# Kernel optimization log

Hardware: AMD Instinct MI355X
Metric: run time of the kernel (lower is better)

## Reference

```python
import jax, jax.numpy as jnp
import numpy as np

DIM = 1536
NH = 24
HD = DIM // NH
EPS = 1e-5


def _ln(x, gamma):
    # LayerNorm over last dim (head_dim), affine weight only, no bias
    mu = jnp.mean(x, axis=-1, keepdims=True)
    var = jnp.var(x, axis=-1, keepdims=True)
    return (x - mu) * jax.lax.rsqrt(var + EPS) * gamma


def setup_inputs() -> dict:
    key = jax.random.key(0)
    ks = jax.random.split(key, 24)
    B, S, T = 1, 2048, 512
    std = 0.02
    d = {
        "hidden_states": jax.random.normal(ks[0], (B, S, DIM), jnp.float32),
        "encoder_hidden_states": jax.random.normal(ks[1], (B, T, DIM), jnp.float32),
        "Wq": jax.random.normal(ks[2], (DIM, DIM), jnp.float32) * std,
        "bq": jnp.zeros((DIM,), jnp.float32),
        "Wk": jax.random.normal(ks[3], (DIM, DIM), jnp.float32) * std,
        "bk": jnp.zeros((DIM,), jnp.float32),
        "Wv": jax.random.normal(ks[4], (DIM, DIM), jnp.float32) * std,
        "bv": jnp.zeros((DIM,), jnp.float32),
        "Waq": jax.random.normal(ks[5], (DIM, DIM), jnp.float32) * std,
        "baq": jnp.zeros((DIM,), jnp.float32),
        "Wak": jax.random.normal(ks[6], (DIM, DIM), jnp.float32) * std,
        "bak": jnp.zeros((DIM,), jnp.float32),
        "Wav": jax.random.normal(ks[7], (DIM, DIM), jnp.float32) * std,
        "bav": jnp.zeros((DIM,), jnp.float32),
        "Wo": jax.random.normal(ks[8], (DIM, DIM), jnp.float32) * std,
        "bo": jnp.zeros((DIM,), jnp.float32),
        "Wao": jax.random.normal(ks[9], (DIM, DIM), jnp.float32) * std,
        "bao": jnp.zeros((DIM,), jnp.float32),
        "gq": jnp.ones((HD,), jnp.float32),
        "gk": jnp.ones((HD,), jnp.float32),
        "gaq": jnp.ones((HD,), jnp.float32),
        "gak": jnp.ones((HD,), jnp.float32),
    }
    return d


def reference(hidden_states, encoder_hidden_states, Wq, bq, Wk, bk, Wv, bv,
              Waq, baq, Wak, bak, Wav, bav, Wo, bo, Wao, bao, gq, gk, gaq, gak):
    B, S, _ = hidden_states.shape
    T = encoder_hidden_states.shape[1]

    def proj(x, W, b):
        # nn.Linear: x @ W.T + b ; reshape to (B, L, NH, HD)
        y = jnp.einsum('bld,ed->ble', x, W) + b
        return y.reshape(B, -1, NH, HD)

    q = _ln(proj(hidden_states, Wq, bq), gq)
    k = _ln(proj(hidden_states, Wk, bk), gk)
    v = proj(hidden_states, Wv, bv)
    eq = _ln(proj(encoder_hidden_states, Waq, baq), gaq)
    ek = _ln(proj(encoder_hidden_states, Wak, bak), gak)
    ev = proj(encoder_hidden_states, Wav, bav)

    q_cat = jnp.concatenate([q, eq], axis=1)  # (B, S+T, H, D)
    k_cat = jnp.concatenate([k, ek], axis=1)
    v_cat = jnp.concatenate([v, ev], axis=1)

    scale = 1.0 / np.sqrt(HD).astype(np.float32)
    scores = jnp.einsum('bqhd,bkhd->bhqk', q_cat, k_cat) * scale
    attn = jax.nn.softmax(scores, axis=-1)
    out = jnp.einsum('bhqk,bkhd->bqhd', attn, v_cat).reshape(B, S + T, DIM)

    img_out = jnp.einsum('bld,ed->ble', out[:, :S], Wo) + bo
    txt_out = jnp.einsum('bld,ed->ble', out[:, S:], Wao) + bao
    return (img_out, txt_out)
```

## Files before the change

kernel.cpp:

```cpp
#include <hip/hip_runtime.h>

#define DIMD 1536
#define LTOT 2560
#define NS 2048
#define NT 512

typedef __bf16 bf16x8 __attribute__((ext_vector_type(8)));
typedef float f32x4 __attribute__((ext_vector_type(4)));
typedef int i32x2 __attribute__((ext_vector_type(2)));
typedef unsigned short u16;
typedef unsigned int u32;

__device__ __forceinline__ u16 f2bf(float f) {
  union { float f; unsigned u; } v; v.f = f;
  return (u16)((v.u + 0x7fffu + ((v.u >> 16) & 1u)) >> 16);
}

__device__ __forceinline__ u32 cvt_pk_bf16(float a, float b) {
  u32 r;
  asm("v_cvt_pk_bf16_f32 %0, %1, %2" : "=v"(r) : "v"(a), "v"(b));
  return r;
}

__device__ __forceinline__ void gload_lds16(const void* g, void* l) {
  __builtin_amdgcn_global_load_lds(
      (__attribute__((address_space(1))) void*)(g),
      (__attribute__((address_space(3))) void*)(l), 16, 0, 0);
}

struct CvtArgs {
  const float* src[10];
  u16* dst[10];
  int n[10];
};

__global__ __launch_bounds__(256) void cvt_all(CvtArgs a) {
  const int seg = blockIdx.y;
  const int n = a.n[seg];
  const float* s = a.src[seg];
  u16* d = a.dst[seg];
  const int i = (blockIdx.x * 256 + threadIdx.x) * 4;
  if (i < n) {
    float4 v = *reinterpret_cast<const float4*>(s + i);
    ushort4 o;
    o.x = f2bf(v.x); o.y = f2bf(v.y); o.z = f2bf(v.z); o.w = f2bf(v.w);
    *reinterpret_cast<ushort4*>(d + i) = o;
  }
}


__device__ __forceinline__ void gemm_stage(const u16* pA, const u16* pW,
                                           u16* As, u16* Bs, int wo) {
#pragma unroll
  for (int p = 0; p < 2; ++p) {
    gload_lds16(pA + (long)p * 64 * DIMD, As + p * 2048 + wo);
    gload_lds16(pW + (long)p * 64 * DIMD, Bs + p * 2048 + wo);
  }
}

__device__ __forceinline__ void gemm_compute(
    const u16* As, const u16* Bs, f32x4 (&acc)[4][4],
    int wr, int wc, int l15, int lh) {
  bf16x8 af[4], bfr[4];
#pragma unroll
  for (int m = 0; m < 4; ++m)
    af[m] = *reinterpret_cast<const bf16x8*>(As + (wr + m * 16 + l15) * 32 + lh * 8);
#pragma unroll
  for (int n = 0; n < 4; ++n)
    bfr[n] = *reinterpret_cast<const bf16x8*>(Bs + (wc + n * 16 + l15) * 32 + lh * 8);
#pragma unroll
  for (int m = 0; m < 4; ++m)
#pragma unroll
    for (int n = 0; n < 4; ++n)
      acc[m][n] = __builtin_amdgcn_mfma_f32_16x16x32_bf16(af[m], bfr[n], acc[m][n], 0, 0, 0);
}

__device__ __forceinline__ void gemm_mainloop(
    const u16* __restrict__ A, const u16* __restrict__ W,
    u16* As0, u16* Bs0, u16* As1, u16* Bs1, f32x4 (&acc)[4][4],
    int w, int lane, int wr, int wc, int l15, int lh) {
  const int base = w * 64 + lane;
  const u16* pA = A + (long)(base >> 2) * DIMD + (base & 3) * 8;
  const u16* pW = W + (long)(base >> 2) * DIMD + (base & 3) * 8;
  const int wo = w * 512;

  gemm_stage(pA, pW, As0, Bs0, wo); pA += 32; pW += 32;
  for (int k0 = 0; k0 < DIMD; k0 += 64) {
    gemm_stage(pA, pW, As1, Bs1, wo); pA += 32; pW += 32;
    asm volatile("s_waitcnt vmcnt(4)" ::: "memory");
    __builtin_amdgcn_s_barrier();
    gemm_compute(As0, Bs0, acc, wr, wc, l15, lh);
    __builtin_amdgcn_s_barrier();
    if (k0 + 64 < DIMD) {
      gemm_stage(pA, pW, As0, Bs0, wo); pA += 32; pW += 32;
      asm volatile("s_waitcnt vmcnt(4)" ::: "memory");
    } else {
      asm volatile("s_waitcnt vmcnt(0)" ::: "memory");
    }
    __builtin_amdgcn_s_barrier();
    gemm_compute(As1, Bs1, acc, wr, wc, l15, lh);
    __builtin_amdgcn_s_barrier();
  }
}

struct QkvArgs {
  const u16* xb; const u16* exb;
  const u16* w[6];
  const float* b[6];
  const float* g[4];
  u16* qcat; u16* kcat; u16* vcat;
};

__global__ __launch_bounds__(256) void qkv_gemm(QkvArgs a) {
  __shared__ u16 As0[128 * 32];
  __shared__ u16 Bs0[128 * 32];
  __shared__ u16 As1[128 * 32];
  __shared__ u16 Bs1[128 * 32];
  const int tid = threadIdx.x, lane = tid & 63, w = tid >> 6;
  const int l15 = lane & 15, lh = lane >> 4;
  const int side = (blockIdx.x >= 16);
  const int mb = side ? (blockIdx.x - 16) : blockIdx.x;
  const int sel = blockIdx.y / 12;
  const int n0 = (blockIdx.y % 12) * 128;
  const long m0 = (long)mb * 128;
  const long Lbase = side ? NS : 0;
  const int wr = (w >> 1) * 64, wc = (w & 1) * 64;
  const u16* A = (side ? a.exb : a.xb) + m0 * DIMD;
  const u16* W = a.w[side * 3 + sel] + (long)n0 * DIMD;
  const float* bias = a.b[side * 3 + sel];

  f32x4 acc[4][4] = {};
  gemm_mainloop(A, W, As0, Bs0, As1, Bs1, acc, w, lane, wr, wc, l15, lh);

  if (sel == 2) {
    u16* out = a.vcat;
#pragma unroll
    for (int m = 0; m < 4; ++m)
#pragma unroll
      for (int r = 0; r < 4; ++r) {
        const long row = Lbase + m0 + wr + m * 16 + lh * 4 + r;
#pragma unroll
        for (int n = 0; n < 4; ++n)
          out[row * DIMD + n0 + wc + n * 16 + l15] =
              f2bf(acc[m][n][r] + bias[n0 + wc + n * 16 + l15]);
      }
  } else {
    const float* gamma = a.g[side * 2 + sel];
    const float gscale = (sel == 0) ? 0.125f * 1.4426950408889634f : 1.0f;
    u16* out = (sel == 0) ? a.qcat : a.kcat;
    const int swz = (sel == 1);
#pragma unroll
    for (int m = 0; m < 4; ++m) {
      float val[4][4];
#pragma unroll
      for (int n = 0; n < 4; ++n) {
        const float b = bias[n0 + wc + n * 16 + l15];
#pragma unroll
        for (int r = 0; r < 4; ++r) val[n][r] = acc[m][n][r] + b;
      }
      float s1[4], s2[4];
#pragma unroll
      for (int r = 0; r < 4; ++r) {
        s1[r] = 0.f; s2[r] = 0.f;
#pragma unroll
        for (int n = 0; n < 4; ++n) { s1[r] += val[n][r]; s2[r] += val[n][r] * val[n][r]; }
      }
#pragma unroll
      for (int off = 1; off < 16; off <<= 1) {
#pragma unroll
        for (int r = 0; r < 4; ++r) {
          s1[r] += __shfl_xor(s1[r], off, 16);
          s2[r] += __shfl_xor(s2[r], off, 16);
        }
      }
#pragma unroll
      for (int r = 0; r < 4; ++r) {
        const float mu = s1[r] * (1.0f / 64.0f);
        const float var = s2[r] * (1.0f / 64.0f) - mu * mu;
        const float rstd = rsqrtf(var + 1e-5f);
        const long row = Lbase + m0 + wr + m * 16 + lh * 4 + r;
        const int r7s = ((lh * 4 + r) & 7) << 3;
#pragma unroll
        for (int n = 0; n < 4; ++n) {
          const float g = gamma[n * 16 + l15] * gscale;
          const int colg = n0 + wc + n * 16 + l15;
          const int colstore = swz ? ((colg & ~63) | ((colg & 63) ^ r7s)) : colg;
          out[row * DIMD + colstore] = f2bf((val[n][r] - mu) * rstd * g);
        }
      }
    }
  }
}

struct OutArgs {
  const u16* aout;
  const u16* w[2];
  const float* b[2];
  float* out;
};

__global__ __launch_bounds__(256) void out_gemm(OutArgs a) {
  __shared__ u16 As0[128 * 32];
  __shared__ u16 Bs0[128 * 32];
  __shared__ u16 As1[128 * 32];
  __shared__ u16 Bs1[128 * 32];
  const int tid = threadIdx.x, lane = tid & 63, w = tid >> 6;
  const int l15 = lane & 15, lh = lane >> 4;
  const int side = (blockIdx.x >= 16);
  const int mb = side ? (blockIdx.x - 16) : blockIdx.x;
  const int n0 = blockIdx.y * 128;
  const long m0 = (long)mb * 128;
  const long Lbase = side ? NS : 0;
  const int wr = (w >> 1) * 64, wc = (w & 1) * 64;
  const u16* A = a.aout + (Lbase + m0) * DIMD;
  const u16* W = a.w[side] + (long)n0 * DIMD;
  const float* bias = a.b[side];

  f32x4 acc[4][4] = {};
  gemm_mainloop(A, W, As0, Bs0, As1, Bs1, acc, w, lane, wr, wc, l15, lh);

#pragma unroll
  for (int m = 0; m < 4; ++m)
#pragma unroll
    for (int r = 0; r < 4; ++r) {
      const long row = Lbase + m0 + wr + m * 16 + lh * 4 + r;
#pragma unroll
      for (int n = 0; n < 4; ++n)
        a.out[row * DIMD + n0 + wc + n * 16 + l15] =
            acc[m][n][r] + bias[n0 + wc + n * 16 + l15];
    }
}

__global__ __launch_bounds__(256) void vtrans(const u16* __restrict__ vcat,
                                              u16* __restrict__ VT) {
  const int tid = threadIdx.x;
  const int kv0 = blockIdx.x * 64;
  const int head = blockIdx.y;
  const long hb = (long)head * 64;
#pragma unroll
  for (int p = 0; p < 2; ++p) {
    const int idx = p * 256 + tid;
    const int kl = idx >> 3, db = (idx & 7) * 8;
    uint4 vv = *reinterpret_cast<const uint4*>(vcat + (long)(kv0 + kl) * DIMD + hb + db);
    const u16* vs = reinterpret_cast<const u16*>(&vv);
#pragma unroll
    for (int i = 0; i < 8; ++i) {
      const int d = db + i;
      VT[(hb + d) * LTOT + ((kv0 + kl) ^ ((d & 7) << 3))] = vs[i];
    }
  }
}


__device__ __forceinline__ void attn_stage(const u16* pK, const u16* pV,
                                           u16* Ks, u16* Vs, int wo) {
#pragma unroll
  for (int ph = 0; ph < 4; ++ph) {
    gload_lds16(pK + (long)ph * 32 * DIMD, Ks + ph * 2048 + wo);
    gload_lds16(pV + (long)ph * 16 * LTOT, Vs + ph * 2048 + wo);
  }
}

__device__ __forceinline__ void attn_tile(
    const u16* Ks, const u16* Vs, const bf16x8 (&aq)[2], bf16x8 ones,
    f32x4 (&oa)[4], f32x4& rs, int l15, int lh, int swl, bool bsel) {
  f32x4 s[8] = {};
#pragma unroll
  for (int c = 0; c < 8; ++c)
#pragma unroll
    for (int kh = 0; kh < 2; ++kh) {
      bf16x8 kb = *reinterpret_cast<const bf16x8*>(
          Ks + (c * 16 + l15) * 64 + ((kh * 32 + lh * 8) ^ swl));
      s[c] = __builtin_amdgcn_mfma_f32_16x16x32_bf16(kb, aq[kh], s[c], 0, 0, 0);
    }

  u32 lo[8], hi[8];
#pragma unroll
  for (int c = 0; c < 8; ++c) {
    lo[c] = cvt_pk_bf16(exp2f(s[c][0]), exp2f(s[c][1]));
    hi[c] = cvt_pk_bf16(exp2f(s[c][2]), exp2f(s[c][3]));
  }

#pragma unroll
  for (int ks = 0; ks < 4; ++ks) {
    i32x2 L = __builtin_amdgcn_permlane32_swap((int)lo[2 * ks], (int)lo[2 * ks + 1], false, false);
    i32x2 H = __builtin_amdgcn_permlane32_swap((int)hi[2 * ks], (int)hi[2 * ks + 1], false, false);
    const int sLy = __shfl_xor(L.y, 16);
    const int sHy = __shfl_xor(H.y, 16);
    const int sLx = __shfl_xor(L.x, 16);
    const int sHx = __shfl_xor(H.x, 16);
    union { int w4[4]; bf16x8 v; } pu;
    pu.w4[0] = bsel ? sLy : L.x;
    pu.w4[1] = bsel ? sHy : H.x;
    pu.w4[2] = bsel ? L.y : sLx;
    pu.w4[3] = bsel ? H.y : sHx;
#pragma unroll
    for (int dg = 0; dg < 4; ++dg) {
      bf16x8 vb = *reinterpret_cast<const bf16x8*>(
          Vs + (dg * 16 + l15) * 128 + ((ks * 32 + lh * 8) ^ swl));
      oa[dg] = __builtin_amdgcn_mfma_f32_16x16x32_bf16(pu.v, vb, oa[dg], 0, 0, 0);
    }
    rs = __builtin_amdgcn_mfma_f32_16x16x32_bf16(pu.v, ones, rs, 0, 0, 0);
  }
}

__global__ __launch_bounds__(256) void flash_attn(
    const u16* __restrict__ Q, const u16* __restrict__ K,
    const u16* __restrict__ VT, u16* __restrict__ O) {
  __shared__ u16 Ks0[128 * 64];
  __shared__ u16 Vs0[64 * 128];
  __shared__ u16 Ks1[128 * 64];
  __shared__ u16 Vs1[64 * 128];
  const int tid = threadIdx.x, lane = tid & 63, w = tid >> 6;
  const int l15 = lane & 15, lh = lane >> 4;
  const bool bsel = lh & 1;
  const long hb = (long)blockIdx.y * 64;
  const long q0 = (long)blockIdx.x * 64 + w * 16;
  const int swl = (l15 & 7) << 3;

  bf16x8 aq[2];
#pragma unroll
  for (int kh = 0; kh < 2; ++kh)
    aq[kh] = *reinterpret_cast<const bf16x8*>(Q + (q0 + l15) * DIMD + hb + kh * 32 + lh * 8);

  union { u32 u[4]; bf16x8 v; } onesu;
#pragma unroll
  for (int i = 0; i < 4; ++i) onesu.u[i] = 0x3F803F80u;

  f32x4 oa[4] = {};
  f32x4 rs = {};

  const u16* pK = K + (long)(tid >> 3) * DIMD + hb + (tid & 7) * 8;
  const u16* pV = VT + (hb + (tid >> 4)) * LTOT + (tid & 15) * 8;
  const int wo = w * 512;

  attn_stage(pK, pV, Ks0, Vs0, wo); pK += (long)128 * DIMD; pV += 128;
  for (int kv0 = 0; kv0 < LTOT; kv0 += 256) {
    attn_stage(pK, pV, Ks1, Vs1, wo); pK += (long)128 * DIMD; pV += 128;
    asm volatile("s_waitcnt vmcnt(8)" ::: "memory");
    __builtin_amdgcn_s_barrier();
    attn_tile(Ks0, Vs0, aq, onesu.v, oa, rs, l15, lh, swl, bsel);
    __builtin_amdgcn_s_barrier();
    if (kv0 + 256 < LTOT) {
      attn_stage(pK, pV, Ks0, Vs0, wo); pK += (long)128 * DIMD; pV += 128;
      asm volatile("s_waitcnt vmcnt(8)" ::: "memory");
    } else {
      asm volatile("s_waitcnt vmcnt(0)" ::: "memory");
    }
    __builtin_amdgcn_s_barrier();
    attn_tile(Ks1, Vs1, aq, onesu.v, oa, rs, l15, lh, swl, bsel);
    __builtin_amdgcn_s_barrier();
  }

#pragma unroll
  for (int r = 0; r < 4; ++r) {
    const float inv = 1.0f / rs[r];
    const long row = q0 + lh * 4 + r;
#pragma unroll
    for (int dg = 0; dg < 4; ++dg)
      O[row * DIMD + hb + dg * 16 + l15] = f2bf(oa[dg][r] * inv);
  }
}

extern "C" void kernel_launch(void* const* d_in, const int* in_sizes, int n_in,
                              void* d_out, int out_size, void* d_ws, size_t ws_size,
                              hipStream_t stream) {
  const float* x   = (const float*)d_in[0];
  const float* ex  = (const float*)d_in[1];
  const float* Wq  = (const float*)d_in[2];  const float* bq  = (const float*)d_in[3];
  const float* Wk  = (const float*)d_in[4];  const float* bk  = (const float*)d_in[5];
  const float* Wv  = (const float*)d_in[6];  const float* bv  = (const float*)d_in[7];
  const float* Waq = (const float*)d_in[8];  const float* baq = (const float*)d_in[9];
  const float* Wak = (const float*)d_in[10]; const float* bak = (const float*)d_in[11];
  const float* Wav = (const float*)d_in[12]; const float* bav = (const float*)d_in[13];
  const float* Wo  = (const float*)d_in[14]; const float* bo  = (const float*)d_in[15];
  const float* Wao = (const float*)d_in[16]; const float* bao = (const float*)d_in[17];
  const float* gq  = (const float*)d_in[18]; const float* gk  = (const float*)d_in[19];
  const float* gaq = (const float*)d_in[20]; const float* gak = (const float*)d_in[21];
  float* out = (float*)d_out;

  u16* ws = (u16*)d_ws;
  const size_t WSZ = (size_t)DIMD * DIMD;
  u16* xb   = ws;
  u16* exb  = xb + (size_t)NS * DIMD;
  u16* wb   = exb + (size_t)NT * DIMD;
  u16* qcat = wb + 8 * WSZ;
  u16* kcat = qcat + (size_t)LTOT * DIMD;
  u16* vcat = kcat + (size_t)LTOT * DIMD;
  u16* VT   = vcat + (size_t)LTOT * DIMD;
  u16* aout = VT + (size_t)LTOT * DIMD;

  CvtArgs ca;
  const float* srcs[10] = {x, ex, Wq, Wk, Wv, Waq, Wak, Wav, Wo, Wao};
  u16* dsts[10] = {xb, exb, wb, wb + WSZ, wb + 2 * WSZ, wb + 3 * WSZ,
                   wb + 4 * WSZ, wb + 5 * WSZ, wb + 6 * WSZ, wb + 7 * WSZ};
  const int ns[10] = {NS * DIMD, NT * DIMD, (int)WSZ, (int)WSZ, (int)WSZ,
                      (int)WSZ, (int)WSZ, (int)WSZ, (int)WSZ, (int)WSZ};
  for (int i = 0; i < 10; ++i) { ca.src[i] = srcs[i]; ca.dst[i] = dsts[i]; ca.n[i] = ns[i]; }
  cvt_all<<<dim3((NS * DIMD) / 1024, 10), 256, 0, stream>>>(ca);

  QkvArgs qa;
  qa.xb = xb; qa.exb = exb;
  qa.w[0] = wb; qa.w[1] = wb + WSZ; qa.w[2] = wb + 2 * WSZ;
  qa.w[3] = wb + 3 * WSZ; qa.w[4] = wb + 4 * WSZ; qa.w[5] = wb + 5 * WSZ;
  qa.b[0] = bq; qa.b[1] = bk; qa.b[2] = bv;
  qa.b[3] = baq; qa.b[4] = bak; qa.b[5] = bav;
  qa.g[0] = gq; qa.g[1] = gk; qa.g[2] = gaq; qa.g[3] = gak;
  qa.qcat = qcat; qa.kcat = kcat; qa.vcat = vcat;
  qkv_gemm<<<dim3(20, 36), 256, 0, stream>>>(qa);

  vtrans<<<dim3(LTOT / 64, 24), 256, 0, stream>>>(vcat, VT);

  flash_attn<<<dim3(LTOT / 64, 24), 256, 0, stream>>>(qcat, kcat, VT, aout);

  OutArgs oa;
  oa.aout = aout;
  oa.w[0] = wb + 6 * WSZ; oa.w[1] = wb + 7 * WSZ;
  oa.b[0] = bo; oa.b[1] = bao;
  oa.out = out;
  out_gemm<<<dim3(20, 12), 256, 0, stream>>>(oa);
}
```

Baseline: 356.7 us.

## Triple-buffer GEMMs, fuse V transpose into QKV epilogue, shrink attention KV tile

The GEMM mainloop moves from double to triple buffering in LDS, so two loads are in flight while one tile is computed. The V projection epilogue writes the swizzled transposed layout directly, which removes the separate vtrans kernel and its extra global round trip. Flash attention changes from 128-key to 64-key tiles, adds s_setprio around compute, uses permlane16_swap where available, and switches to a hardware exp2 builtin. The trade-off is more LDS per GEMM block, which may lower occupancy, and scattered 2-byte stores in the V epilogue.

```diff
diff --git a/kernel.cpp b/kernel.cpp
--- a/kernel.cpp
+++ b/kernel.cpp
@@ -10,6 +10,12 @@
 typedef int i32x2 __attribute__((ext_vector_type(2)));
 typedef unsigned short u16;
 typedef unsigned int u32;
+
+#if __has_builtin(__builtin_amdgcn_exp2f)
+#define EXP2(x) __builtin_amdgcn_exp2f(x)
+#else
+#define EXP2(x) exp2f(x)
+#endif
 
 __device__ __forceinline__ u16 f2bf(float f) {
   union { float f; unsigned u; } v; v.f = f;
@@ -51,11 +57,10 @@
 
 __device__ __forceinline__ void gemm_stage(const u16* pA, const u16* pW,
                                            u16* As, u16* Bs, int wo) {
-#pragma unroll
-  for (int p = 0; p < 2; ++p) {
-    gload_lds16(pA + (long)p * 64 * DIMD, As + p * 2048 + wo);
-    gload_lds16(pW + (long)p * 64 * DIMD, Bs + p * 2048 + wo);
-  }
+  gload_lds16(pA, As + wo);
+  gload_lds16(pA + (long)64 * DIMD, As + 2048 + wo);
+  gload_lds16(pW, Bs + wo);
+  gload_lds16(pW + (long)64 * DIMD, Bs + 2048 + wo);
 }
 
 __device__ __forceinline__ void gemm_compute(
@@ -75,32 +80,43 @@
       acc[m][n] = __builtin_amdgcn_mfma_f32_16x16x32_bf16(af[m], bfr[n], acc[m][n], 0, 0, 0);
 }
 
+#define VMW(N) asm volatile("s_waitcnt vmcnt(" #N ")" ::: "memory")
+#define BAR() __builtin_amdgcn_s_barrier()
+
 __device__ __forceinline__ void gemm_mainloop(
     const u16* __restrict__ A, const u16* __restrict__ W,
-    u16* As0, u16* Bs0, u16* As1, u16* Bs1, f32x4 (&acc)[4][4],
-    int w, int lane, int wr, int wc, int l15, int lh) {
-  const int base = w * 64 + lane;
-  const u16* pA = A + (long)(base >> 2) * DIMD + (base & 3) * 8;
-  const u16* pW = W + (long)(base >> 2) * DIMD + (base & 3) * 8;
+    u16* As0, u16* Bs0, u16* As1, u16* Bs1, u16* As2, u16* Bs2,
+    f32x4 (&acc)[4][4], int w, int lane, int wr, int wc, int l15, int lh) {
+  const int tid = w * 64 + lane;
+  const u16* pA = A + (long)(tid >> 2) * DIMD + (tid & 3) * 8;
+  const u16* pW = W + (long)(tid >> 2) * DIMD + (tid & 3) * 8;
   const int wo = w * 512;
 
   gemm_stage(pA, pW, As0, Bs0, wo); pA += 32; pW += 32;
-  for (int k0 = 0; k0 < DIMD; k0 += 64) {
+  gemm_stage(pA, pW, As1, Bs1, wo); pA += 32; pW += 32;
+  for (int i = 0; i < 15; ++i) {
+    gemm_stage(pA, pW, As2, Bs2, wo); pA += 32; pW += 32;
+    VMW(8); BAR();
+    gemm_compute(As0, Bs0, acc, wr, wc, l15, lh);
+    BAR();
+    gemm_stage(pA, pW, As0, Bs0, wo); pA += 32; pW += 32;
+    VMW(8); BAR();
+    gemm_compute(As1, Bs1, acc, wr, wc, l15, lh);
+    BAR();
     gemm_stage(pA, pW, As1, Bs1, wo); pA += 32; pW += 32;
-    asm volatile("s_waitcnt vmcnt(4)" ::: "memory");
-    __builtin_amdgcn_s_barrier();
-    gemm_compute(As0, Bs0, acc, wr, wc, l15, lh);
-    __builtin_amdgcn_s_barrier();
-    if (k0 + 64 < DIMD) {
-      gemm_stage(pA, pW, As0, Bs0, wo); pA += 32; pW += 32;
-      asm volatile("s_waitcnt vmcnt(4)" ::: "memory");
-    } else {
-      asm volatile("s_waitcnt vmcnt(0)" ::: "memory");
-    }
-    __builtin_amdgcn_s_barrier();
-    gemm_compute(As1, Bs1, acc, wr, wc, l15, lh);
-    __builtin_amdgcn_s_barrier();
-  }
+    VMW(8); BAR();
+    gemm_compute(As2, Bs2, acc, wr, wc, l15, lh);
+    BAR();
+  }
+  gemm_stage(pA, pW, As2, Bs2, wo);
+  VMW(8); BAR();
+  gemm_compute(As0, Bs0, acc, wr, wc, l15, lh);
+  BAR();
+  VMW(4); BAR();
+  gemm_compute(As1, Bs1, acc, wr, wc, l15, lh);
+  BAR();
+  VMW(0); BAR();
+  gemm_compute(As2, Bs2, acc, wr, wc, l15, lh);
 }
 
 struct QkvArgs {
@@ -108,7 +124,7 @@
   const u16* w[6];
   const float* b[6];
   const float* g[4];
-  u16* qcat; u16* kcat; u16* vcat;
+  u16* qcat; u16* kcat; u16* VT;
 };
 
 __global__ __launch_bounds__(256) void qkv_gemm(QkvArgs a) {
@@ -116,6 +132,8 @@
   __shared__ u16 Bs0[128 * 32];
   __shared__ u16 As1[128 * 32];
   __shared__ u16 Bs1[128 * 32];
+  __shared__ u16 As2[128 * 32];
+  __shared__ u16 Bs2[128 * 32];
   const int tid = threadIdx.x, lane = tid & 63, w = tid >> 6;
   const int l15 = lane & 15, lh = lane >> 4;
   const int side = (blockIdx.x >= 16);
@@ -130,19 +148,21 @@
   const float* bias = a.b[side * 3 + sel];
 
   f32x4 acc[4][4] = {};
-  gemm_mainloop(A, W, As0, Bs0, As1, Bs1, acc, w, lane, wr, wc, l15, lh);
+  gemm_mainloop(A, W, As0, Bs0, As1, Bs1, As2, Bs2, acc, w, lane, wr, wc, l15, lh);
 
   if (sel == 2) {
-    u16* out = a.vcat;
+    u16* VT = a.VT;
 #pragma unroll
     for (int m = 0; m < 4; ++m)
 #pragma unroll
       for (int r = 0; r < 4; ++r) {
-        const long row = Lbase + m0 + wr + m * 16 + lh * 4 + r;
-#pragma unroll
-        for (int n = 0; n < 4; ++n)
-          out[row * DIMD + n0 + wc + n * 16 + l15] =
-              f2bf(acc[m][n][r] + bias[n0 + wc + n * 16 + l15]);
+        const int row = (int)(Lbase + m0) + wr + m * 16 + lh * 4 + r;
+#pragma unroll
+        for (int n = 0; n < 4; ++n) {
+          const int col = n0 + wc + n * 16 + l15;
+          const float v = acc[m][n][r] + bias[col];
+          VT[(long)col * LTOT + (row ^ ((col & 7) << 3))] = f2bf(v);
+        }
       }
   } else {
     const float* gamma = a.g[side * 2 + sel];
@@ -204,6 +224,8 @@
   __shared__ u16 Bs0[128 * 32];
   __shared__ u16 As1[128 * 32];
   __shared__ u16 Bs1[128 * 32];
+  __shared__ u16 As2[128 * 32];
+  __shared__ u16 Bs2[128 * 32];
   const int tid = threadIdx.x, lane = tid & 63, w = tid >> 6;
   const int l15 = lane & 15, lh = lane >> 4;
   const int side = (blockIdx.x >= 16);
@@ -217,7 +239,7 @@
   const float* bias = a.b[side];
 
   f32x4 acc[4][4] = {};
-  gemm_mainloop(A, W, As0, Bs0, As1, Bs1, acc, w, lane, wr, wc, l15, lh);
+  gemm_mainloop(A, W, As0, Bs0, As1, Bs1, As2, Bs2, acc, w, lane, wr, wc, l15, lh);
 
 #pragma unroll
   for (int m = 0; m < 4; ++m)
@@ -231,42 +253,21 @@
     }
 }
 
-__global__ __launch_bounds__(256) void vtrans(const u16* __restrict__ vcat,
-                                              u16* __restrict__ VT) {
-  const int tid = threadIdx.x;
-  const int kv0 = blockIdx.x * 64;
-  const int head = blockIdx.y;
-  const long hb = (long)head * 64;
-#pragma unroll
-  for (int p = 0; p < 2; ++p) {
-    const int idx = p * 256 + tid;
-    const int kl = idx >> 3, db = (idx & 7) * 8;
-    uint4 vv = *reinterpret_cast<const uint4*>(vcat + (long)(kv0 + kl) * DIMD + hb + db);
-    const u16* vs = reinterpret_cast<const u16*>(&vv);
-#pragma unroll
-    for (int i = 0; i < 8; ++i) {
-      const int d = db + i;
-      VT[(hb + d) * LTOT + ((kv0 + kl) ^ ((d & 7) << 3))] = vs[i];
-    }
-  }
-}
-
 
 __device__ __forceinline__ void attn_stage(const u16* pK, const u16* pV,
                                            u16* Ks, u16* Vs, int wo) {
-#pragma unroll
-  for (int ph = 0; ph < 4; ++ph) {
-    gload_lds16(pK + (long)ph * 32 * DIMD, Ks + ph * 2048 + wo);
-    gload_lds16(pV + (long)ph * 16 * LTOT, Vs + ph * 2048 + wo);
-  }
+  gload_lds16(pK, Ks + wo);
+  gload_lds16(pK + (long)32 * DIMD, Ks + 2048 + wo);
+  gload_lds16(pV, Vs + wo);
+  gload_lds16(pV + (long)32 * LTOT, Vs + 2048 + wo);
 }
 
 __device__ __forceinline__ void attn_tile(
     const u16* Ks, const u16* Vs, const bf16x8 (&aq)[2], bf16x8 ones,
     f32x4 (&oa)[4], f32x4& rs, int l15, int lh, int swl, bool bsel) {
-  f32x4 s[8] = {};
-#pragma unroll
-  for (int c = 0; c < 8; ++c)
+  f32x4 s[4] = {};
+#pragma unroll
+  for (int c = 0; c < 4; ++c)
 #pragma unroll
     for (int kh = 0; kh < 2; ++kh) {
       bf16x8 kb = *reinterpret_cast<const bf16x8*>(
@@ -274,30 +275,36 @@
       s[c] = __builtin_amdgcn_mfma_f32_16x16x32_bf16(kb, aq[kh], s[c], 0, 0, 0);
     }
 
-  u32 lo[8], hi[8];
-#pragma unroll
-  for (int c = 0; c < 8; ++c) {
-    lo[c] = cvt_pk_bf16(exp2f(s[c][0]), exp2f(s[c][1]));
-    hi[c] = cvt_pk_bf16(exp2f(s[c][2]), exp2f(s[c][3]));
-  }
-
-#pragma unroll
-  for (int ks = 0; ks < 4; ++ks) {
+  u32 lo[4], hi[4];
+#pragma unroll
+  for (int c = 0; c < 4; ++c) {
+    lo[c] = cvt_pk_bf16(EXP2(s[c][0]), EXP2(s[c][1]));
+    hi[c] = cvt_pk_bf16(EXP2(s[c][2]), EXP2(s[c][3]));
+  }
+
+#pragma unroll
+  for (int ks = 0; ks < 2; ++ks) {
     i32x2 L = __builtin_amdgcn_permlane32_swap((int)lo[2 * ks], (int)lo[2 * ks + 1], false, false);
     i32x2 H = __builtin_amdgcn_permlane32_swap((int)hi[2 * ks], (int)hi[2 * ks + 1], false, false);
+    union { int w4[4]; bf16x8 v; } pu;
+#if __has_builtin(__builtin_amdgcn_permlane16_swap)
+    i32x2 W02 = __builtin_amdgcn_permlane16_swap(L.x, L.y, false, false);
+    i32x2 W13 = __builtin_amdgcn_permlane16_swap(H.x, H.y, false, false);
+    pu.w4[0] = W02.x; pu.w4[1] = W13.x; pu.w4[2] = W02.y; pu.w4[3] = W13.y;
+#else
     const int sLy = __shfl_xor(L.y, 16);
     const int sHy = __shfl_xor(H.y, 16);
     const int sLx = __shfl_xor(L.x, 16);
     const int sHx = __shfl_xor(H.x, 16);
-    union { int w4[4]; bf16x8 v; } pu;
     pu.w4[0] = bsel ? sLy : L.x;
     pu.w4[1] = bsel ? sHy : H.x;
     pu.w4[2] = bsel ? L.y : sLx;
     pu.w4[3] = bsel ? H.y : sHx;
+#endif
 #pragma unroll
     for (int dg = 0; dg < 4; ++dg) {
       bf16x8 vb = *reinterpret_cast<const bf16x8*>(
-          Vs + (dg * 16 + l15) * 128 + ((ks * 32 + lh * 8) ^ swl));
+          Vs + (dg * 16 + l15) * 64 + ((ks * 32 + lh * 8) ^ swl));
       oa[dg] = __builtin_amdgcn_mfma_f32_16x16x32_bf16(pu.v, vb, oa[dg], 0, 0, 0);
     }
     rs = __builtin_amdgcn_mfma_f32_16x16x32_bf16(pu.v, ones, rs, 0, 0, 0);
@@ -307,10 +314,10 @@
 __global__ __launch_bounds__(256) void flash_attn(
     const u16* __restrict__ Q, const u16* __restrict__ K,
     const u16* __restrict__ VT, u16* __restrict__ O) {
-  __shared__ u16 Ks0[128 * 64];
-  __shared__ u16 Vs0[64 * 128];
-  __shared__ u16 Ks1[128 * 64];
-  __shared__ u16 Vs1[64 * 128];
+  __shared__ u16 Ks0[64 * 64];
+  __shared__ u16 Vs0[64 * 64];
+  __shared__ u16 Ks1[64 * 64];
+  __shared__ u16 Vs1[64 * 64];
   const int tid = threadIdx.x, lane = tid & 63, w = tid >> 6;
   const int l15 = lane & 15, lh = lane >> 4;
   const bool bsel = lh & 1;
@@ -331,25 +338,31 @@
   f32x4 rs = {};
 
   const u16* pK = K + (long)(tid >> 3) * DIMD + hb + (tid & 7) * 8;
-  const u16* pV = VT + (hb + (tid >> 4)) * LTOT + (tid & 15) * 8;
+  const u16* pV = VT + (hb + (tid >> 3)) * LTOT + (tid & 7) * 8;
   const int wo = w * 512;
 
-  attn_stage(pK, pV, Ks0, Vs0, wo); pK += (long)128 * DIMD; pV += 128;
-  for (int kv0 = 0; kv0 < LTOT; kv0 += 256) {
-    attn_stage(pK, pV, Ks1, Vs1, wo); pK += (long)128 * DIMD; pV += 128;
-    asm volatile("s_waitcnt vmcnt(8)" ::: "memory");
-    __builtin_amdgcn_s_barrier();
+  attn_stage(pK, pV, Ks0, Vs0, wo);
+  pK += (long)64 * DIMD; pV += 64;
+  for (int t = 0; t < 40; t += 2) {
+    attn_stage(pK, pV, Ks1, Vs1, wo);
+    pK += (long)64 * DIMD; pV += 64;
+    VMW(4); BAR();
+    __builtin_amdgcn_s_setprio(1);
     attn_tile(Ks0, Vs0, aq, onesu.v, oa, rs, l15, lh, swl, bsel);
-    __builtin_amdgcn_s_barrier();
-    if (kv0 + 256 < LTOT) {
-      attn_stage(pK, pV, Ks0, Vs0, wo); pK += (long)128 * DIMD; pV += 128;
-      asm volatile("s_waitcnt vmcnt(8)" ::: "memory");
+    __builtin_amdgcn_s_setprio(0);
+    BAR();
+    if (t + 2 < 40) {
+      attn_stage(pK, pV, Ks0, Vs0, wo);
+      pK += (long)64 * DIMD; pV += 64;
+      VMW(4);
     } else {
-      asm volatile("s_waitcnt vmcnt(0)" ::: "memory");
+      VMW(0);
     }
-    __builtin_amdgcn_s_barrier();
+    BAR();
+    __builtin_amdgcn_s_setprio(1);
     attn_tile(Ks1, Vs1, aq, onesu.v, oa, rs, l15, lh, swl, bsel);
-    __builtin_amdgcn_s_barrier();
+    __builtin_amdgcn_s_setprio(0);
+    BAR();
   }
 
 #pragma unroll
@@ -386,8 +399,7 @@
   u16* wb   = exb + (size_t)NT * DIMD;
   u16* qcat = wb + 8 * WSZ;
   u16* kcat = qcat + (size_t)LTOT * DIMD;
-  u16* vcat = kcat + (size_t)LTOT * DIMD;
-  u16* VT   = vcat + (size_t)LTOT * DIMD;
+  u16* VT   = kcat + (size_t)LTOT * DIMD;
   u16* aout = VT + (size_t)LTOT * DIMD;
 
   CvtArgs ca;
@@ -406,10 +418,8 @@
   qa.b[0] = bq; qa.b[1] = bk; qa.b[2] = bv;
   qa.b[3] = baq; qa.b[4] = bak; qa.b[5] = bav;
   qa.g[0] = gq; qa.g[1] = gk; qa.g[2] = gaq; qa.g[3] = gak;
-  qa.qcat = qcat; qa.kcat = kcat; qa.vcat = vcat;
+  qa.qcat = qcat; qa.kcat = kcat; qa.VT = VT;
   qkv_gemm<<<dim3(20, 36), 256, 0, stream>>>(qa);
-
-  vtrans<<<dim3(LTOT / 64, 24), 256, 0, stream>>>(vcat, VT);
 
   flash_attn<<<dim3(LTOT / 64, 24), 256, 0, stream>>>(qcat, kcat, VT, aout);
 
```

After: 316.5 us. -11.3%, faster.
